# Performance work log

Hardware: AMD Instinct MI355X
Metric: run time of the kernel (lower is better)

The kernel has to match this reference:

```python
import jax, jax.numpy as jnp
import numpy as np

# QuantumConv2d from ESPCN-PyTorch (quantum variant).
# QuantumLinear(kH, kW, ...) is a parameterized quantum circuit mapping a flattened
# kH*kW patch to kH Z-expectation values. We model the standard single-qubit-per-row
# RY-chain circuit: out[k] = cos( sum_w patch[k, w] + theta[k] )  (Z expectation after
# sequential RY rotations by the kW row inputs plus one trainable angle per row).
# The conv then averages the kH outputs and sums over input channels, exactly as the
# torch forward does. We replicate the original's circuits[i*j] indexing (i=out ch,
# j=in ch), and use cos(a+b)=cos a cos b - sin a sin b to turn the channel/row
# reduction into two dense einsums (same math, efficient expression).

KH, KW = 3, 3
PH, PW = 1, 1
OC = 32


def setup_inputs() -> dict:
    key = jax.random.key(0)
    k1, k2 = jax.random.split(key)
    x = jax.random.normal(k1, (8, 16, 128, 128), dtype=jnp.float32)
    # one circuit per (out_ch, in_ch, kernel_row): oC*iC*kH = 32*16*3 = 1536, kH params each
    theta = jax.random.normal(k2, (OC * 16 * KH, KH), dtype=jnp.float32)
    return {"x": x, "theta": theta}


def _row_window_sums(x):
    # x: (n, iC, H, W) -> (n, iC, kH, oH, oW): sum over the kW window for each kernel row
    xp = jnp.pad(x, ((0, 0), (0, 0), (PH, PH), (PW, PW)))
    Hp, Wp = xp.shape[2], xp.shape[3]
    oH, oW = Hp - (KH - 1), Wp - (KW - 1)
    rows = []
    for k in range(KH):  # tiny fixed loop over kernel rows
        s = xp[:, :, k:k + oH, 0:oW]
        for w in range(1, KW):
            s = s + xp[:, :, k:k + oH, w:w + oW]
        rows.append(s)
    return jnp.stack(rows, axis=2)


def reference(x, theta):
    n, iC = x.shape[0], x.shape[1]
    R = _row_window_sums(x)  # (n, iC, kH, oH, oW) angle sums per patch row
    # replicate torch's self.circuits[i * j] lookup
    idx = jnp.arange(OC)[:, None] * jnp.arange(iC)[None, :]  # (oC, iC)
    th = theta[idx]  # (oC, iC, kH)
    # out[n,i,h,w] = sum_j mean_k cos(R[n,j,k,h,w] + th[i,j,k])
    out = (jnp.einsum('njkhw,ijk->nihw', jnp.cos(R), jnp.cos(th))
           - jnp.einsum('njkhw,ijk->nihw', jnp.sin(R), jnp.sin(th))) / KH
    return out
```

## Files before the change

### kernel.cpp

```cpp
#include <hip/hip_runtime.h>

#define OC 32
#define IC 16
#define HH 128
#define WW 128
#define NB 8
#define RP 130
#define TRIG_DW (NB * RP * WW * IC)
#define A_OFF TRIG_DW
#define A_DW (OC * 48)
#define TOTAL_DW (TRIG_DW + A_DW)

typedef __attribute__((ext_vector_type(8))) __bf16 bf16x8;
typedef __attribute__((ext_vector_type(4))) float f32x4;
typedef __attribute__((ext_vector_type(4))) unsigned int u32x4;

#define INV_2PI 0.15915494309189535f

__device__ inline unsigned int pack2bf(float lo, float hi) {
    union { __bf16 h[2]; unsigned int u; } p;
    p.h[0] = (__bf16)lo;
    p.h[1] = (__bf16)hi;
    return p.u;
}

__device__ inline void hw_sincos(float rad, float* sn, float* cs) {
    float rev = rad * INV_2PI;
    float fr = rev - floorf(rev);
    *sn = __builtin_amdgcn_sinf(fr);
    *cs = __builtin_amdgcn_cosf(fr);
}

__global__ void trig_kernel(const float* __restrict__ x,
                            const float* __restrict__ theta,
                            unsigned int* __restrict__ ws) {
    int idx = blockIdx.x * 256 + threadIdx.x;
    if (idx >= TOTAL_DW) return;

    if (idx < TRIG_DW) {
        int j  = idx & 15;
        int w  = (idx >> 4) & (WW - 1);
        int t3 = idx >> 11;
        int rp = t3 % RP;
        int n  = t3 / RP;
        int r  = rp - 1;
        unsigned int pk = 0x00003F80u;
        if (r >= 0 && r < HH) {
            const float* row = x + ((size_t)(n * IC + j) * HH + r) * WW;
            float c0 = row[w];
            float cm = (w > 0)      ? row[w - 1] : 0.f;
            float cp = (w < WW - 1) ? row[w + 1] : 0.f;
            float s = cm + c0 + cp;
            float sn, cs;
            hw_sincos(s, &sn, &cs);
            pk = pack2bf(cs, sn);
        }
        ws[idx] = pk;
    } else {
        int q  = idx - A_OFF;
        int oc = q / 48;
        int mp = q - oc * 48;
        int kk = mp >> 4;
        int j  = mp & 15;
        float th = theta[(oc * j) * 3 + kk];
        float sn, cs;
        hw_sincos(th, &sn, &cs);
        const float inv3 = 1.0f / 3.0f;
        ws[idx] = pack2bf(cs * inv3, -sn * inv3);
    }
}

__global__ __launch_bounds__(256, 4) void gemm_kernel(
        const unsigned int* __restrict__ ws,
        float* __restrict__ out) {
    const int tx = threadIdx.x;
    const int ty = threadIdx.y;

    const int bid = blockIdx.x;
    const int wbase = (bid & 1) * 64;
    const int hp = (bid >> 1) & 63;
    const int n  = bid >> 7;
    const int h0 = hp * 2;

    const int l15 = tx & 15;
    const int lk  = tx >> 4;

    union U4 { u32x4 v; bf16x8 h; };

    bf16x8 afr[3][2];
#pragma unroll
    for (int Kt = 0; Kt < 3; ++Kt)
#pragma unroll
        for (int Mt = 0; Mt < 2; ++Mt) {
            U4 a;
            a.v = *(const u32x4*)(ws + A_OFF + (l15 + 16 * Mt) * 48 + Kt * 16 + lk * 4);
            afr[Kt][Mt] = a.h;
        }

    bf16x8 bfr[3][2];
#pragma unroll
    for (int Nt = 0; Nt < 2; ++Nt) {
        int px = ty * 32 + 16 * Nt + l15;
        int hrow = px >> 6;
        int w = wbase + (px & 63);
#pragma unroll
        for (int Kt = 0; Kt < 3; ++Kt) {
            int rp = h0 + hrow + Kt;
            U4 b;
            b.v = *(const u32x4*)(ws + ((size_t)(n * RP + rp) * WW + w) * 16 + lk * 4);
            bfr[Kt][Nt] = b.h;
        }
    }

    f32x4 acc[2][2];
#pragma unroll
    for (int a = 0; a < 2; ++a)
#pragma unroll
        for (int b = 0; b < 2; ++b) acc[a][b] = (f32x4){0.f, 0.f, 0.f, 0.f};

#pragma unroll
    for (int Kt = 0; Kt < 3; ++Kt)
#pragma unroll
        for (int Mt = 0; Mt < 2; ++Mt)
#pragma unroll
            for (int Nt = 0; Nt < 2; ++Nt)
                acc[Mt][Nt] = __builtin_amdgcn_mfma_f32_16x16x32_bf16(
                    afr[Kt][Mt], bfr[Kt][Nt], acc[Mt][Nt], 0, 0, 0);

#pragma unroll
    for (int Mt = 0; Mt < 2; ++Mt)
#pragma unroll
        for (int Nt = 0; Nt < 2; ++Nt)
#pragma unroll
            for (int e = 0; e < 4; ++e) {
                int oc = 16 * Mt + lk * 4 + e;
                int px = ty * 32 + 16 * Nt + l15;
                int hrow = px >> 6, wloc = px & 63;
                out[(((size_t)n * OC + oc) * HH + (h0 + hrow)) * WW + (wbase + wloc)]
                    = acc[Mt][Nt][e];
            }
}

extern "C" void kernel_launch(void* const* d_in, const int* in_sizes, int n_in,
                              void* d_out, int out_size, void* d_ws, size_t ws_size,
                              hipStream_t stream) {
    const float* x     = (const float*)d_in[0];
    const float* theta = (const float*)d_in[1];
    float* out = (float*)d_out;
    unsigned int* ws = (unsigned int*)d_ws;

    trig_kernel<<<(TOTAL_DW + 255) / 256, 256, 0, stream>>>(x, theta, ws);

    dim3 block(64, 4, 1);
    gemm_kernel<<<NB * (HH / 2) * 2, block, 0, stream>>>(ws, out);
}
```

Measured before the change: 81.96 us.

## Coalesce trig kernel reads via per-row blocks with LDS transpose

The trig kernel now gives each block one padded row of one image. Threads read x along w, which is the contiguous axis in memory, for each channel, so global loads become coalesced; the old per-dword mapping made lanes stride across channels. Results are transposed through padded shared memory into the channel-innermost workspace layout and written as 16-byte vector stores. Theta preprocessing moves to one extra block, and padding rows are filled with vector stores. The cost is a __syncthreads and the LDS use per block.

```diff
diff --git a/kernel.cpp b/kernel.cpp
--- a/kernel.cpp
+++ b/kernel.cpp
@@ -31,43 +31,67 @@
     *cs = __builtin_amdgcn_cosf(fr);
 }
 
-__global__ void trig_kernel(const float* __restrict__ x,
-                            const float* __restrict__ theta,
-                            unsigned int* __restrict__ ws) {
-    int idx = blockIdx.x * 256 + threadIdx.x;
-    if (idx >= TOTAL_DW) return;
+__global__ __launch_bounds__(256) void trig_kernel(
+        const float* __restrict__ x,
+        const float* __restrict__ theta,
+        unsigned int* __restrict__ ws) {
+    __shared__ unsigned int T[128 * 17];
 
-    if (idx < TRIG_DW) {
-        int j  = idx & 15;
-        int w  = (idx >> 4) & (WW - 1);
-        int t3 = idx >> 11;
-        int rp = t3 % RP;
-        int n  = t3 / RP;
-        int r  = rp - 1;
-        unsigned int pk = 0x00003F80u;
-        if (r >= 0 && r < HH) {
-            const float* row = x + ((size_t)(n * IC + j) * HH + r) * WW;
-            float c0 = row[w];
-            float cm = (w > 0)      ? row[w - 1] : 0.f;
-            float cp = (w < WW - 1) ? row[w + 1] : 0.f;
-            float s = cm + c0 + cp;
+    const int bid = blockIdx.x;
+    const int t = threadIdx.x;
+
+    if (bid == NB * RP) {
+        const float inv3 = 1.0f / 3.0f;
+        for (int q = t; q < OC * 48; q += 256) {
+            int oc = q / 48;
+            int mp = q - oc * 48;
+            int kk = mp >> 4;
+            int j  = mp & 15;
+            float th = theta[(oc * j) * 3 + kk];
             float sn, cs;
-            hw_sincos(s, &sn, &cs);
-            pk = pack2bf(cs, sn);
+            hw_sincos(th, &sn, &cs);
+            ws[A_OFF + q] = pack2bf(cs * inv3, -sn * inv3);
         }
-        ws[idx] = pk;
-    } else {
-        int q  = idx - A_OFF;
-        int oc = q / 48;
-        int mp = q - oc * 48;
-        int kk = mp >> 4;
-        int j  = mp & 15;
-        float th = theta[(oc * j) * 3 + kk];
+        return;
+    }
+
+    const int n  = bid / RP;
+    const int rp = bid - n * RP;
+    const int r  = rp - 1;
+    unsigned int* dst = ws + (size_t)bid * 2048;
+
+    if (r < 0 || r >= HH) {
+        u32x4 v = (u32x4){0x3F80u, 0x3F80u, 0x3F80u, 0x3F80u};
+        *(u32x4*)(dst + t * 8)     = v;
+        *(u32x4*)(dst + t * 8 + 4) = v;
+        return;
+    }
+
+    const int w  = t & 127;
+    const int jr = t >> 7;
+    const float* xr = x + ((size_t)n * IC * HH + r) * WW;
+    const bool wl = (w > 0), wrk = (w < WW - 1);
+#pragma unroll
+    for (int it = 0; it < 8; ++it) {
+        int j = it * 2 + jr;
+        const float* row = xr + (size_t)j * (HH * WW);
+        float c0 = row[w];
+        float cm = wl  ? row[w - 1] : 0.f;
+        float cp = wrk ? row[w + 1] : 0.f;
+        float s = cm + c0 + cp;
         float sn, cs;
-        hw_sincos(th, &sn, &cs);
-        const float inv3 = 1.0f / 3.0f;
-        ws[idx] = pack2bf(cs * inv3, -sn * inv3);
+        hw_sincos(s, &sn, &cs);
+        T[w * 17 + j] = pack2bf(cs, sn);
     }
+    __syncthreads();
+
+    const int wo = t >> 1;
+    const int jh = (t & 1) * 8;
+    unsigned int vals[8];
+#pragma unroll
+    for (int e = 0; e < 8; ++e) vals[e] = T[wo * 17 + jh + e];
+    *(u32x4*)(dst + t * 8)     = (u32x4){vals[0], vals[1], vals[2], vals[3]};
+    *(u32x4*)(dst + t * 8 + 4) = (u32x4){vals[4], vals[5], vals[6], vals[7]};
 }
 
 __global__ __launch_bounds__(256, 4) void gemm_kernel(
@@ -149,7 +173,7 @@
     float* out = (float*)d_out;
     unsigned int* ws = (unsigned int*)d_ws;
 
-    trig_kernel<<<(TOTAL_DW + 255) / 256, 256, 0, stream>>>(x, theta, ws);
+    trig_kernel<<<NB * RP + 1, 256, 0, stream>>>(x, theta, ws);
 
     dim3 block(64, 4, 1);
     gemm_kernel<<<NB * (HH / 2) * 2, block, 0, stream>>>(ws, out);
```

Result: faster. 75.39 us (-8.0%).
